# Kernel tuning notes

Hardware: AMD Instinct MI355X
Metric: run time of the kernel (lower is better)

## Reference

```python
import jax, jax.numpy as jnp
import numpy as np

NUM_USERS = 10000
NUM_ITEMS = 100000
EMBED_DIM = 64
BATCH = 4096


def setup_inputs() -> dict:
    key = jax.random.key(0)
    k1, k2, k3, k4, k5 = jax.random.split(key, 5)
    user_emb = jax.random.normal(k1, (NUM_USERS, EMBED_DIM), dtype=jnp.float32)
    item_emb = jax.random.normal(k2, (NUM_ITEMS, EMBED_DIM), dtype=jnp.float32)
    social_weight = jax.random.normal(k3, (NUM_USERS, NUM_USERS), dtype=jnp.float32)
    users = jax.random.randint(k4, (BATCH,), 0, NUM_USERS, dtype=jnp.int64)
    items = jax.random.randint(k5, (BATCH,), 0, NUM_ITEMS, dtype=jnp.int64)
    return {"user_emb": user_emb, "item_emb": item_emb,
            "social_weight": social_weight, "users": users, "items": items}


def reference(user_emb, item_emb, social_weight, users, items):
    # Embedding gathers
    bu = user_emb[users]            # [B, D]
    bi = item_emb[items]            # [B, D]
    # Per-sample dot product (bmm of [B,1,D] x [B,D,1] in the original)
    pos = jnp.sum(bu * bi, axis=-1)                      # [B]
    # Social branch. Original tiles user table B times and does bmm:
    #   scores[b] = user_emb @ bi[b]  -> [B, U]; one matmul, no replication.
    social_scores = jnp.einsum('bd,ud->bu', bi, user_emb)  # [B, U]
    bw = social_weight[users]                              # [B, U]
    social_influence = jnp.sum(bw * social_scores, axis=-1)  # [B]
    return pos + social_influence
```

## Files before the change

### kernel.cpp

```cpp
#include <hip/hip_runtime.h>
#include <hip/hip_bf16.h>

#define NUSERS   10000
#define NITEMS   100000
#define DIM      64
#define BATCH    4096

#define KPAD     10240
#define SPC      16
#define NCHUNK   20
#define MT       64

typedef __bf16 bf16_t;
typedef __bf16 bf16x8 __attribute__((ext_vector_type(8)));
typedef float  f32x4  __attribute__((ext_vector_type(4)));

__global__ void prep_ueT_kernel(const float* __restrict__ user_emb,
                                bf16_t* __restrict__ ueT) {
    int d = blockIdx.y;
    int k = blockIdx.x * 256 + threadIdx.x;
    float v = (k < NUSERS) ? user_emb[(size_t)k * DIM + d] : 0.0f;
    ueT[(size_t)d * KPAD + k] = (bf16_t)v;
}

__global__ void pos_kernel(const float* __restrict__ user_emb,
                           const float* __restrict__ item_emb,
                           const int* __restrict__ users,
                           const int* __restrict__ items,
                           float* __restrict__ out) {
    int w    = threadIdx.x >> 6;
    int lane = threadIdx.x & 63;
    int b    = blockIdx.x * 4 + w;
    if (b >= BATCH) return;
    int uid = users[b];
    int iid = items[b];
    float v = user_emb[(size_t)uid * DIM + lane] * item_emb[(size_t)iid * DIM + lane];
    v += __shfl_xor(v, 32, 64);
    v += __shfl_xor(v, 16, 64);
    v += __shfl_xor(v, 8, 64);
    v += __shfl_xor(v, 4, 64);
    v += __shfl_xor(v, 2, 64);
    v += __shfl_xor(v, 1, 64);
    if (lane == 0) out[b] = v;
}

__global__ __launch_bounds__(256) void social_kernel(
        const float* __restrict__ sw,
        const bf16_t* __restrict__ ueT,
        const float* __restrict__ item_emb,
        const int* __restrict__ users,
        const int* __restrict__ items,
        float* __restrict__ out) {
    const int tid  = threadIdx.x;
    const int w    = tid >> 6;
    const int lane = tid & 63;
    const int q    = lane >> 4;
    const int c    = lane & 15;

    const int m0   = blockIdx.y * MT;
    const int arow = m0 + 16 * w + c;
    const int uid  = users[arow];
    const float*  ap  = sw + (size_t)uid * NUSERS;
    const bf16_t* bp0 = ueT + (size_t)(c     ) * KPAD;
    const bf16_t* bp1 = ueT + (size_t)(c + 16) * KPAD;
    const bf16_t* bp2 = ueT + (size_t)(c + 32) * KPAD;
    const bf16_t* bp3 = ueT + (size_t)(c + 48) * KPAD;

    f32x4 acc0 = {0.f, 0.f, 0.f, 0.f};
    f32x4 acc1 = {0.f, 0.f, 0.f, 0.f};
    f32x4 acc2 = {0.f, 0.f, 0.f, 0.f};
    f32x4 acc3 = {0.f, 0.f, 0.f, 0.f};

    int k = blockIdx.x * (SPC * 32) + 8 * q;

    #pragma unroll 2
    for (int s = 0; s < SPC; ++s, k += 32) {
        float4 a0 = {0.f, 0.f, 0.f, 0.f};
        float4 a1 = {0.f, 0.f, 0.f, 0.f};
        if (k < NUSERS) {
            const float4* p = (const float4*)(ap + k);
            a0 = p[0];
            a1 = p[1];
        }
        const bf16x8 b0 = *(const bf16x8*)(bp0 + k);
        const bf16x8 b1 = *(const bf16x8*)(bp1 + k);
        const bf16x8 b2 = *(const bf16x8*)(bp2 + k);
        const bf16x8 b3 = *(const bf16x8*)(bp3 + k);

        bf16x8 av;
        av[0] = (bf16_t)a0.x; av[1] = (bf16_t)a0.y;
        av[2] = (bf16_t)a0.z; av[3] = (bf16_t)a0.w;
        av[4] = (bf16_t)a1.x; av[5] = (bf16_t)a1.y;
        av[6] = (bf16_t)a1.z; av[7] = (bf16_t)a1.w;

        acc0 = __builtin_amdgcn_mfma_f32_16x16x32_bf16(av, b0, acc0, 0, 0, 0);
        acc1 = __builtin_amdgcn_mfma_f32_16x16x32_bf16(av, b1, acc1, 0, 0, 0);
        acc2 = __builtin_amdgcn_mfma_f32_16x16x32_bf16(av, b2, acc2, 0, 0, 0);
        acc3 = __builtin_amdgcn_mfma_f32_16x16x32_bf16(av, b3, acc3, 0, 0, 0);
    }

    for (int r = 0; r < 4; ++r) {
        const int grow = m0 + 16 * w + 4 * q + r;
        const int iid  = items[grow];
        const float* ie = item_emb + (size_t)iid * DIM;
        float v = acc0[r] * ie[c]
                + acc1[r] * ie[c + 16]
                + acc2[r] * ie[c + 32]
                + acc3[r] * ie[c + 48];
        v += __shfl_xor(v, 1, 64);
        v += __shfl_xor(v, 2, 64);
        v += __shfl_xor(v, 4, 64);
        v += __shfl_xor(v, 8, 64);
        if (c == 0) atomicAdd(out + grow, v);
    }
}

extern "C" void kernel_launch(void* const* d_in, const int* in_sizes, int n_in,
                              void* d_out, int out_size, void* d_ws, size_t ws_size,
                              hipStream_t stream) {
    const float* user_emb = (const float*)d_in[0];
    const float* item_emb = (const float*)d_in[1];
    const float* sw       = (const float*)d_in[2];
    const int*   users    = (const int*)d_in[3];
    const int*   items    = (const int*)d_in[4];
    float* out = (float*)d_out;

    bf16_t* ueT = (bf16_t*)d_ws;

    prep_ueT_kernel<<<dim3(KPAD / 256, DIM), 256, 0, stream>>>(user_emb, ueT);

    pos_kernel<<<BATCH / 4, 256, 0, stream>>>(user_emb, item_emb, users, items, out);

    social_kernel<<<dim3(NCHUNK, BATCH / MT), 256, 0, stream>>>(
        sw, ueT, item_emb, users, items, out);
}
```

Measured before the change: 513.1 us.

## Fuse prep and pos kernels, transpose via LDS tile, rebalance K chunks

Merges the user-embedding transpose/convert kernel and the positive-score kernel into one launch, with block ranges split between the two roles. The transpose now does coalesced float4 reads and writes through a padded shared-memory tile instead of strided per-element reads. The social kernel's K split changes from 20 chunks of 16 steps to 16 chunks of 20 steps, giving fewer atomics and larger per-block work but fewer blocks. The total runtime is dominated by streaming the social-weight rows, so the gain is likely modest.

```diff
diff --git a/kernel.cpp b/kernel.cpp
--- a/kernel.cpp
+++ b/kernel.cpp
@@ -7,41 +7,74 @@
 #define BATCH    4096
 
 #define KPAD     10240
-#define SPC      16
-#define NCHUNK   20
+#define SPC      20
+#define NCHUNK   16
 #define MT       64
+
+#define PREP_BLOCKS (KPAD / 64)
+#define POS_BLOCKS  (BATCH / 4)
 
 typedef __bf16 bf16_t;
 typedef __bf16 bf16x8 __attribute__((ext_vector_type(8)));
 typedef float  f32x4  __attribute__((ext_vector_type(4)));
 
-__global__ void prep_ueT_kernel(const float* __restrict__ user_emb,
-                                bf16_t* __restrict__ ueT) {
-    int d = blockIdx.y;
-    int k = blockIdx.x * 256 + threadIdx.x;
-    float v = (k < NUSERS) ? user_emb[(size_t)k * DIM + d] : 0.0f;
-    ueT[(size_t)d * KPAD + k] = (bf16_t)v;
-}
+__global__ __launch_bounds__(256) void prep_pos_kernel(
+        const float* __restrict__ user_emb,
+        const float* __restrict__ item_emb,
+        const int* __restrict__ users,
+        const int* __restrict__ items,
+        bf16_t* __restrict__ ueT,
+        float* __restrict__ out) {
+    __shared__ bf16_t tile[64 * 72];
 
-__global__ void pos_kernel(const float* __restrict__ user_emb,
-                           const float* __restrict__ item_emb,
-                           const int* __restrict__ users,
-                           const int* __restrict__ items,
-                           float* __restrict__ out) {
-    int w    = threadIdx.x >> 6;
-    int lane = threadIdx.x & 63;
-    int b    = blockIdx.x * 4 + w;
-    if (b >= BATCH) return;
-    int uid = users[b];
-    int iid = items[b];
-    float v = user_emb[(size_t)uid * DIM + lane] * item_emb[(size_t)iid * DIM + lane];
-    v += __shfl_xor(v, 32, 64);
-    v += __shfl_xor(v, 16, 64);
-    v += __shfl_xor(v, 8, 64);
-    v += __shfl_xor(v, 4, 64);
-    v += __shfl_xor(v, 2, 64);
-    v += __shfl_xor(v, 1, 64);
-    if (lane == 0) out[b] = v;
+    const int tid = threadIdx.x;
+
+    if (blockIdx.x < PREP_BLOCKS) {
+        const int k0  = blockIdx.x * 64;
+        const int r   = tid >> 2;
+        const int seg = tid & 3;
+        const int krow = k0 + r;
+
+        float4 f0 = {0.f,0.f,0.f,0.f}, f1 = f0, f2 = f0, f3 = f0;
+        if (krow < NUSERS) {
+            const float4* p = (const float4*)(user_emb + (size_t)krow * DIM + 16 * seg);
+            f0 = p[0]; f1 = p[1]; f2 = p[2]; f3 = p[3];
+        }
+        bf16x8 v0, v1;
+        v0[0]=(bf16_t)f0.x; v0[1]=(bf16_t)f0.y; v0[2]=(bf16_t)f0.z; v0[3]=(bf16_t)f0.w;
+        v0[4]=(bf16_t)f1.x; v0[5]=(bf16_t)f1.y; v0[6]=(bf16_t)f1.z; v0[7]=(bf16_t)f1.w;
+        v1[0]=(bf16_t)f2.x; v1[1]=(bf16_t)f2.y; v1[2]=(bf16_t)f2.z; v1[3]=(bf16_t)f2.w;
+        v1[4]=(bf16_t)f3.x; v1[5]=(bf16_t)f3.y; v1[6]=(bf16_t)f3.z; v1[7]=(bf16_t)f3.w;
+        *(bf16x8*)(tile + r * 72 + 16 * seg)     = v0;
+        *(bf16x8*)(tile + r * 72 + 16 * seg + 8) = v1;
+        __syncthreads();
+
+        const int d    = tid >> 2;
+        const int kseg = tid & 3;
+        bf16x8 o0, o1;
+        #pragma unroll
+        for (int i = 0; i < 8; ++i) {
+            o0[i] = tile[(16 * kseg + i    ) * 72 + d];
+            o1[i] = tile[(16 * kseg + i + 8) * 72 + d];
+        }
+        bf16_t* dst = ueT + (size_t)d * KPAD + k0 + 16 * kseg;
+        *(bf16x8*)(dst)     = o0;
+        *(bf16x8*)(dst + 8) = o1;
+    } else {
+        const int w    = tid >> 6;
+        const int lane = tid & 63;
+        const int b    = (blockIdx.x - PREP_BLOCKS) * 4 + w;
+        const int uid = users[b];
+        const int iid = items[b];
+        float v = user_emb[(size_t)uid * DIM + lane] * item_emb[(size_t)iid * DIM + lane];
+        v += __shfl_xor(v, 32, 64);
+        v += __shfl_xor(v, 16, 64);
+        v += __shfl_xor(v, 8, 64);
+        v += __shfl_xor(v, 4, 64);
+        v += __shfl_xor(v, 2, 64);
+        v += __shfl_xor(v, 1, 64);
+        if (lane == 0) out[b] = v;
+    }
 }
 
 __global__ __launch_bounds__(256) void social_kernel(
@@ -127,9 +160,8 @@
 
     bf16_t* ueT = (bf16_t*)d_ws;
 
-    prep_ueT_kernel<<<dim3(KPAD / 256, DIM), 256, 0, stream>>>(user_emb, ueT);
-
-    pos_kernel<<<BATCH / 4, 256, 0, stream>>>(user_emb, item_emb, users, items, out);
+    prep_pos_kernel<<<PREP_BLOCKS + POS_BLOCKS, 256, 0, stream>>>(
+        user_emb, item_emb, users, items, ueT, out);
 
     social_kernel<<<dim3(NCHUNK, BATCH / MT), 256, 0, stream>>>(
         sw, ueT, item_emb, users, items, out);
```

After: 499.4 us. 2.7% less time.
